# Optimization experiments

Hardware: AMD Instinct MI355X
Metric: run time of the kernel (lower is better)

## Reference

```python
import jax, jax.numpy as jnp
import numpy as np
from jax import lax

B, S, I, H = 128, 256, 512, 1024


def setup_inputs() -> dict:
    key = jax.random.key(0)
    ks = jax.random.split(key, 7)
    s_att = 1.0 / np.sqrt(I + H)
    s_ih = 1.0 / np.sqrt(H)
    return {
        "x": jax.random.normal(ks[0], (B, S, I), dtype=jnp.float32),
        "W_att": jax.random.uniform(ks[1], (1, I + H), minval=-s_att, maxval=s_att, dtype=jnp.float32),
        "b_att": jax.random.uniform(ks[2], (1,), minval=-s_att, maxval=s_att, dtype=jnp.float32),
        "W_ih": jax.random.uniform(ks[3], (3 * H, I), minval=-s_ih, maxval=s_ih, dtype=jnp.float32),
        "W_hh": jax.random.uniform(ks[4], (3 * H, H), minval=-s_ih, maxval=s_ih, dtype=jnp.float32),
        "b_ih": jax.random.uniform(ks[5], (3 * H,), minval=-s_ih, maxval=s_ih, dtype=jnp.float32),
        "b_hh": jax.random.uniform(ks[6], (3 * H,), minval=-s_ih, maxval=s_ih, dtype=jnp.float32),
    }


def reference(x, W_att, b_att, W_ih, W_hh, b_ih, b_hh):
    batch, seq_len, _ = x.shape
    hid = W_hh.shape[1]

    def step(h, x_t):
        # attention score over the BATCH dim (faithful to softmax(dim=0) on [B,1])
        score = jnp.concatenate([x_t, h], axis=1) @ W_att.T + b_att  # [B,1]
        att = jax.nn.softmax(score, axis=0)
        x_att = att * x_t  # [B,I]
        # PyTorch GRUCell: gates in order r, z, n
        gi = x_att @ W_ih.T + b_ih  # [B,3H]
        gh = h @ W_hh.T + b_hh      # [B,3H]
        i_r, i_z, i_n = jnp.split(gi, 3, axis=1)
        h_r, h_z, h_n = jnp.split(gh, 3, axis=1)
        r = jax.nn.sigmoid(i_r + h_r)
        z = jax.nn.sigmoid(i_z + h_z)
        n = jnp.tanh(i_n + r * h_n)
        h_new = (1.0 - z) * n + z * h
        return h_new, h_new

    h0 = jnp.zeros((batch, hid), dtype=x.dtype)
    xs = jnp.swapaxes(x, 0, 1)  # [S,B,I]
    h_last, outs = lax.scan(step, h0, xs)  # outs: [S,B,H]
    outputs = jnp.swapaxes(outs, 0, 1)  # [B,S,H]
    return outputs, h_last
```

## Files before the change

### kernel.cpp

```cpp
#include <hip/hip_runtime.h>
#include <hip/hip_bf16.h>

#define B_ 128
#define S_ 256
#define I_ 512
#define H_ 1024

typedef float  f32x4  __attribute__((ext_vector_type(4)));
typedef __bf16 bf16x8 __attribute__((ext_vector_type(8)));
typedef unsigned short u16x8 __attribute__((ext_vector_type(8)));

__device__ __forceinline__ unsigned short f2bf(float f) {
    unsigned u = __float_as_uint(f);
    unsigned r = (u + 0x7fffu + ((u >> 16) & 1u)) >> 16;
    return (unsigned short)r;
}
__device__ __forceinline__ float bf2f(unsigned short s) {
    return __uint_as_float(((unsigned)s) << 16);
}


__global__ __launch_bounds__(256) void pack_wih(const float* __restrict__ W,
                                                unsigned short* __restrict__ out) {
    int gid = blockIdx.x * 256 + threadIdx.x;
    int lane = gid & 63, ks = (gid >> 6) & 15, p = gid >> 10;
    int c = lane & 15, quad = lane >> 4;
    int k = ks * 32 + quad * 8;
    int n = 0; bool valid = true;
    if (c < 4) n = p * 4 + c;
    else if (c < 8) n = H_ + p * 4 + (c - 4);
    else if (c < 12) n = 2 * H_ + p * 4 + (c - 8);
    else valid = false;
    const float* src = W + (size_t)n * I_ + k;
    u16x8 v;
#pragma unroll
    for (int jj = 0; jj < 8; jj++) v[jj] = valid ? f2bf(src[jj]) : (unsigned short)0;
    *(u16x8*)(out + (size_t)gid * 8) = v;
}

__global__ __launch_bounds__(256) void pack_whh(const float* __restrict__ W,
                                                const float* __restrict__ Watt,
                                                unsigned short* __restrict__ hi,
                                                unsigned short* __restrict__ lo) {
    int gid = blockIdx.x * 256 + threadIdx.x;
    int lane = gid & 63, ks = (gid >> 6) & 31, p = gid >> 11;
    int c = lane & 15, quad = lane >> 4;
    int k = ks * 32 + quad * 8;
    u16x8 vh, vl;
#pragma unroll
    for (int jj = 0; jj < 8; jj++) {
        float f = 0.f;
        if (c < 4)        f = W[(size_t)(p * 4 + c) * H_ + k + jj];
        else if (c < 8)   f = W[(size_t)(H_ + p * 4 + (c - 4)) * H_ + k + jj];
        else if (c < 12)  f = W[(size_t)(2 * H_ + p * 4 + (c - 8)) * H_ + k + jj];
        else if (c == 12) f = Watt[I_ + k + jj];
        unsigned short h16 = f2bf(f);
        unsigned short l16 = f2bf(f - bf2f(h16));
        vh[jj] = h16; vl[jj] = l16;
    }
    *(u16x8*)(hi + (size_t)gid * 8) = vh;
    *(u16x8*)(lo + (size_t)gid * 8) = vl;
}

__global__ __launch_bounds__(256) void pack_x(const float* __restrict__ x,
                                              unsigned short* __restrict__ Gx) {
    int bid = blockIdx.x;
    int t = bid >> 3, m = bid & 7;
    int tid = threadIdx.x;
    __shared__ unsigned short tile[16 * 520];
#pragma unroll
    for (int pass = 0; pass < 8; pass++) {
        int idx = pass * 256 + tid;
        int row = idx >> 7, c4 = idx & 127;
        float4 v = *(const float4*)(x + ((size_t)(m * 16 + row) * S_ + t) * I_ + c4 * 4);
        unsigned short* d = &tile[row * 520 + c4 * 4];
        d[0] = f2bf(v.x); d[1] = f2bf(v.y); d[2] = f2bf(v.z); d[3] = f2bf(v.w);
    }
    __syncthreads();
#pragma unroll
    for (int pass = 0; pass < 4; pass++) {
        int chunk = pass * 256 + tid;
        int ks = chunk >> 6, lane = chunk & 63;
        int c = lane & 15, kq = lane >> 4;
        int k = ks * 32 + kq * 8;
        u16x8 v = *(const u16x8*)(&tile[c * 520 + k]);
        *(u16x8*)(Gx + (((size_t)(t * 8 + m) * 16 + ks) * 64 + lane) * 8) = v;
    }
}

__global__ __launch_bounds__(256) void sx_kernel(const float* __restrict__ x,
                                                 const float* __restrict__ Watt,
                                                 float* __restrict__ sx) {
    int t = blockIdx.x;
    int w = threadIdx.x >> 6, lane = threadIdx.x & 63;
    float4 wa0 = *(const float4*)(Watt + lane * 8);
    float4 wa1 = *(const float4*)(Watt + lane * 8 + 4);
    for (int i = 0; i < 32; i++) {
        int b = w * 32 + i;
        const float4* xp = (const float4*)(x + ((size_t)b * S_ + t) * I_ + lane * 8);
        float4 a0 = xp[0], a1 = xp[1];
        float s = a0.x * wa0.x + a0.y * wa0.y + a0.z * wa0.z + a0.w * wa0.w
                + a1.x * wa1.x + a1.y * wa1.y + a1.z * wa1.z + a1.w * wa1.w;
#pragma unroll
        for (int off = 1; off < 64; off <<= 1) s += __shfl_xor(s, off, 64);
        if (lane == 0) sx[t * 128 + b] = s;
    }
}

__global__ __launch_bounds__(512, 2) void gru_persist(
        const unsigned short* __restrict__ Gx,
        const float* __restrict__ sx,
        const unsigned short* __restrict__ WihP,
        const unsigned short* __restrict__ WhhHiP,
        const unsigned short* __restrict__ WhhLoP,
        unsigned short* __restrict__ Hhi,
        unsigned short* __restrict__ Hlo,
        const float* __restrict__ batt,
        const float* __restrict__ bih, const float* __restrict__ bhh,
        float* __restrict__ out, unsigned* __restrict__ bar) {
    int p = blockIdx.x;
    int tid = threadIdx.x, w = tid >> 6, lane = tid & 63;
    int quad = lane >> 4, c = lane & 15, cl = c & 3;

    __shared__ unsigned short bhi[16384];
    __shared__ unsigned short blo[16384];
    __shared__ unsigned short wih_lds[8192];
    __shared__ float sh_lds[128];
    __shared__ float score_lds[128];

    {
        const uint4* s0 = (const uint4*)(WhhHiP + (size_t)p * 16384);
        uint4* d0 = (uint4*)bhi;
        for (int i = tid; i < 2048; i += 512) d0[i] = s0[i];
        const uint4* s1 = (const uint4*)(WhhLoP + (size_t)p * 16384);
        uint4* d1 = (uint4*)blo;
        for (int i = tid; i < 2048; i += 512) d1[i] = s1[i];
        const uint4* s2 = (const uint4*)(WihP + (size_t)p * 8192);
        uint4* d2 = (uint4*)wih_lds;
        for (int i = tid; i < 1024; i += 512) d2[i] = s2[i];
    }
    float ba = batt[0];
    int j = p * 4 + cl;
    float bihr = bih[j], bihz = bih[H_ + j], bihn = bih[2 * H_ + j];
    float bhhr = bhh[j], bhhz = bhh[H_ + j], bhhn = bhh[2 * H_ + j];
    __syncthreads();

    float hprev[4] = {0.f, 0.f, 0.f, 0.f};
    int k32 = (p & 7) * 4 + cl;
    int j_e = k32 & 7;
    size_t chunk_base = ((size_t)w * 32 + (size_t)(p >> 3)) * 64
                      + (size_t)(quad * 4) + 16 * (size_t)(k32 >> 3);

    for (int t = 0; t < S_; t++) {
        const unsigned short* hchi = Hhi + (size_t)t * 131072;
        const unsigned short* hclo = Hlo + (size_t)t * 131072;
        unsigned* hnhi32 = (unsigned*)(Hhi + (size_t)(t + 1) * 131072);
        unsigned* hnlo32 = (unsigned*)(Hlo + (size_t)(t + 1) * 131072);
        float sxv = (tid < 128) ? sx[t * 128 + tid] : 0.f;

        const unsigned short* ahb = hchi + (size_t)w * 16384 + (size_t)lane * 8;
        const unsigned short* alb = hclo + (size_t)w * 16384 + (size_t)lane * 8;
        const unsigned short* xab = Gx + (size_t)t * 65536 + (size_t)w * 8192
                                       + (size_t)lane * 8;

        u16x8 ph[8], pl8[8], px[8];
#pragma unroll
        for (int s = 0; s < 8; s++) {
            ph[s]  = *(const u16x8*)(ahb + s * 512);
            pl8[s] = *(const u16x8*)(alb + s * 512);
            px[s]  = *(const u16x8*)(xab + s * 512);
        }

        f32x4 accg = (f32x4){0.f, 0.f, 0.f, 0.f};
        f32x4 acc0 = (f32x4){0.f, 0.f, 0.f, 0.f};
        f32x4 acc1 = (f32x4){0.f, 0.f, 0.f, 0.f};
#pragma unroll
        for (int ks = 0; ks < 32; ks++) {
            const int s = ks & 7;
            bf16x8 ah = __builtin_bit_cast(bf16x8, ph[s]);
            bf16x8 al = __builtin_bit_cast(bf16x8, pl8[s]);
            bf16x8 bh = *(const bf16x8*)(bhi + ((size_t)ks * 64 + lane) * 8);
            bf16x8 bl = *(const bf16x8*)(blo + ((size_t)ks * 64 + lane) * 8);
            if (ks < 16) {
                bf16x8 xa = __builtin_bit_cast(bf16x8, px[s]);
                bf16x8 wb = *(const bf16x8*)(wih_lds + ((size_t)ks * 64 + lane) * 8);
                accg = __builtin_amdgcn_mfma_f32_16x16x32_bf16(xa, wb, accg, 0, 0, 0);
                if (ks + 8 < 16) px[s] = *(const u16x8*)(xab + (ks + 8) * 512);
            }
            if (ks & 1) {
                acc1 = __builtin_amdgcn_mfma_f32_16x16x32_bf16(ah, bh, acc1, 0, 0, 0);
                acc1 = __builtin_amdgcn_mfma_f32_16x16x32_bf16(al, bh, acc1, 0, 0, 0);
                acc1 = __builtin_amdgcn_mfma_f32_16x16x32_bf16(ah, bl, acc1, 0, 0, 0);
            } else {
                acc0 = __builtin_amdgcn_mfma_f32_16x16x32_bf16(ah, bh, acc0, 0, 0, 0);
                acc0 = __builtin_amdgcn_mfma_f32_16x16x32_bf16(al, bh, acc0, 0, 0, 0);
                acc0 = __builtin_amdgcn_mfma_f32_16x16x32_bf16(ah, bl, acc0, 0, 0, 0);
            }
            if (ks + 8 < 32) {
                ph[s]  = *(const u16x8*)(ahb + (ks + 8) * 512);
                pl8[s] = *(const u16x8*)(alb + (ks + 8) * 512);
            }
        }

        f32x4 gh;
#pragma unroll
        for (int r = 0; r < 4; r++) gh[r] = acc0[r] + acc1[r];
        if (c == 12) {
#pragma unroll
            for (int r = 0; r < 4; r++) sh_lds[w * 16 + quad * 4 + r] = gh[r];
        }
        __syncthreads();
        if (tid < 128) score_lds[tid] = sh_lds[tid] + sxv + ba;
        __syncthreads();

        float s0 = score_lds[lane], s1 = score_lds[lane + 64];
        float mx = fmaxf(s0, s1);
#pragma unroll
        for (int off = 1; off < 64; off <<= 1) mx = fmaxf(mx, __shfl_xor(mx, off, 64));
        float pe = __expf(s0 - mx) + __expf(s1 - mx);
#pragma unroll
        for (int off = 1; off < 64; off <<= 1) pe += __shfl_xor(pe, off, 64);
        float rden = 1.f / pe;

#pragma unroll
        for (int r = 0; r < 4; r++) {
            int b = w * 16 + quad * 4 + r;
            float att = __expf(score_lds[b] - mx) * rden;
            float ghr = gh[r];
            float ghz = __shfl_xor(ghr, 4, 64);
            float ghn = __shfl_xor(ghr, 8, 64);
            float gir = accg[r];
            float giz = __shfl_xor(gir, 4, 64);
            float gin = __shfl_xor(gir, 8, 64);
            float rg = 1.f / (1.f + __expf(-(att * gir + bihr + ghr + bhhr)));
            float zg = 1.f / (1.f + __expf(-(att * giz + bihz + ghz + bhhz)));
            float ta = att * gin + bihn + rg * (ghn + bhhn);
            ta = fminf(fmaxf(ta, -15.f), 15.f);
            float e2 = __expf(2.f * ta);
            float ng = (e2 - 1.f) / (e2 + 1.f);
            float hnew = (1.f - zg) * ng + zg * hprev[r];
            hprev[r] = hnew;
            if (c < 4) {
                out[((size_t)b * S_ + t) * H_ + j] = hnew;
                unsigned short hi16 = f2bf(hnew);
                unsigned short lo16 = f2bf(hnew - bf2f(hi16));
                unsigned hval = (unsigned)hi16 | ((unsigned)lo16 << 16);
                unsigned nb = __shfl_xor(hval, 1, 64);
                if (!(cl & 1)) {
                    unsigned hipair = (hval & 0xffffu) | (nb << 16);
                    unsigned lopair = (hval >> 16) | (nb & 0xffff0000u);
                    unsigned* dh = hnhi32 + (chunk_base + r) * 4 + (j_e >> 1);
                    unsigned* dl = hnlo32 + (chunk_base + r) * 4 + (j_e >> 1);
                    asm volatile("global_store_dword %0, %1, off sc0 sc1"
                                 :: "v"(dh), "v"(hipair) : "memory");
                    asm volatile("global_store_dword %0, %1, off sc0 sc1"
                                 :: "v"(dl), "v"(lopair) : "memory");
                }
            }
        }

        if (t + 1 < S_) {
            __syncthreads();
            if (tid < 64) {
                if (lane == 0)
                    __hip_atomic_fetch_add(bar + (p & 7) * 32, 1u,
                                           __ATOMIC_RELAXED, __HIP_MEMORY_SCOPE_AGENT);
                unsigned tgt = (unsigned)(t + 1) * 32u;
                for (;;) {
                    unsigned v = tgt;
                    if (lane < 8)
                        v = __hip_atomic_load(bar + lane * 32, __ATOMIC_RELAXED,
                                              __HIP_MEMORY_SCOPE_AGENT);
                    if (__all(v >= tgt)) break;
                    __builtin_amdgcn_s_sleep(1);
                }
            }
            __syncthreads();
        }
    }

    if (c < 4) {
#pragma unroll
        for (int r = 0; r < 4; r++)
            out[(size_t)B_ * S_ * H_ + (size_t)(w * 16 + quad * 4 + r) * H_ + j] = hprev[r];
    }
}

extern "C" void kernel_launch(void* const* d_in, const int* in_sizes, int n_in,
                              void* d_out, int out_size, void* d_ws, size_t ws_size,
                              hipStream_t stream) {
    (void)in_sizes; (void)n_in; (void)out_size; (void)ws_size;
    const float* x    = (const float*)d_in[0];
    const float* Watt = (const float*)d_in[1];
    const float* batt = (const float*)d_in[2];
    const float* Wih  = (const float*)d_in[3];
    const float* Whh  = (const float*)d_in[4];
    const float* bih  = (const float*)d_in[5];
    const float* bhh  = (const float*)d_in[6];
    float* out = (float*)d_out;

    char* ws = (char*)d_ws;
    size_t off = 0;
    unsigned short* Gx     = (unsigned short*)(ws + off); off += 33554432ULL;
    unsigned short* WihP   = (unsigned short*)(ws + off); off += 4194304ULL;
    unsigned short* WhhHiP = (unsigned short*)(ws + off); off += 8388608ULL;
    unsigned short* WhhLoP = (unsigned short*)(ws + off); off += 8388608ULL;
    float*          sx     = (float*)(ws + off);          off += 131072ULL;
    unsigned short* Hhi    = (unsigned short*)(ws + off); off += 67371008ULL;
    unsigned short* Hlo    = (unsigned short*)(ws + off); off += 67371008ULL;
    unsigned*       bar    = (unsigned*)(ws + off);       off += 1024ULL;

    hipMemsetAsync(Hhi, 0, 262144, stream);
    hipMemsetAsync(Hlo, 0, 262144, stream);
    hipMemsetAsync(bar, 0, 1024, stream);
    pack_wih<<<1024, 256, 0, stream>>>(Wih, WihP);
    pack_whh<<<2048, 256, 0, stream>>>(Whh, Watt, WhhHiP, WhhLoP);
    pack_x<<<2048, 256, 0, stream>>>(x, Gx);
    sx_kernel<<<256, 256, 0, stream>>>(x, Watt, sx);
    gru_persist<<<256, 512, 0, stream>>>(Gx, sx, WihP, WhhHiP, WhhLoP, Hhi, Hlo,
                                         batt, bih, bhh, out, bar);
}
```

Measured before the change: 3.264 ms.

## Split recurrent K-loop across two wave groups with 1024-thread blocks

Doubles the block to 1024 threads. The lower 8 waves compute the first half of the W_hh K-reduction, and the upper 8 waves compute the second half plus the input-gate MFMAs. Partial sums are combined through LDS before the softmax and gate epilogue. The next step's x tile and sx value are prefetched after the current step's compute to shorten the serial per-step critical path. The cost is an extra LDS exchange and barrier, higher register pressure from launch_bounds(1024,4), and upper waves sitting idle during the epilogue.

```diff
diff --git a/kernel.cpp b/kernel.cpp
--- a/kernel.cpp
+++ b/kernel.cpp
@@ -107,7 +107,7 @@
     }
 }
 
-__global__ __launch_bounds__(512, 2) void gru_persist(
+__global__ __launch_bounds__(1024, 4) void gru_persist(
         const unsigned short* __restrict__ Gx,
         const float* __restrict__ sx,
         const unsigned short* __restrict__ WihP,
@@ -119,30 +119,36 @@
         const float* __restrict__ bih, const float* __restrict__ bhh,
         float* __restrict__ out, unsigned* __restrict__ bar) {
     int p = blockIdx.x;
-    int tid = threadIdx.x, w = tid >> 6, lane = tid & 63;
+    int tid = threadIdx.x, w16 = tid >> 6, lane = tid & 63;
+    const bool upper = (w16 >= 8);
+    int w = upper ? (w16 - 8) : w16;
     int quad = lane >> 4, c = lane & 15, cl = c & 3;
 
     __shared__ unsigned short bhi[16384];
     __shared__ unsigned short blo[16384];
     __shared__ unsigned short wih_lds[8192];
+    __shared__ f32x4 part_gh[8][64];
+    __shared__ f32x4 part_gi[8][64];
     __shared__ float sh_lds[128];
     __shared__ float score_lds[128];
 
     {
         const uint4* s0 = (const uint4*)(WhhHiP + (size_t)p * 16384);
         uint4* d0 = (uint4*)bhi;
-        for (int i = tid; i < 2048; i += 512) d0[i] = s0[i];
+        for (int i = tid; i < 2048; i += 1024) d0[i] = s0[i];
         const uint4* s1 = (const uint4*)(WhhLoP + (size_t)p * 16384);
         uint4* d1 = (uint4*)blo;
-        for (int i = tid; i < 2048; i += 512) d1[i] = s1[i];
+        for (int i = tid; i < 2048; i += 1024) d1[i] = s1[i];
         const uint4* s2 = (const uint4*)(WihP + (size_t)p * 8192);
-        uint4* d2 = (uint4*)wih_lds;
-        for (int i = tid; i < 1024; i += 512) d2[i] = s2[i];
+        ((uint4*)wih_lds)[tid] = s2[tid];
     }
     float ba = batt[0];
     int j = p * 4 + cl;
-    float bihr = bih[j], bihz = bih[H_ + j], bihn = bih[2 * H_ + j];
-    float bhhr = bhh[j], bhhz = bhh[H_ + j], bhhn = bhh[2 * H_ + j];
+    float bihr = 0.f, bihz = 0.f, bihn = 0.f, bhhr = 0.f, bhhz = 0.f, bhhn = 0.f;
+    if (!upper) {
+        bihr = bih[j]; bihz = bih[H_ + j]; bihn = bih[2 * H_ + j];
+        bhhr = bhh[j]; bhhz = bhh[H_ + j]; bhhn = bhh[2 * H_ + j];
+    }
     __syncthreads();
 
     float hprev[4] = {0.f, 0.f, 0.f, 0.f};
@@ -151,112 +157,170 @@
     size_t chunk_base = ((size_t)w * 32 + (size_t)(p >> 3)) * 64
                       + (size_t)(quad * 4) + 16 * (size_t)(k32 >> 3);
 
+    u16x8 px[8];
+    if (upper) {
+        const unsigned short* xab0 = Gx + (size_t)w * 8192 + (size_t)lane * 8;
+#pragma unroll
+        for (int s = 0; s < 8; s++) px[s] = *(const u16x8*)(xab0 + s * 512);
+    }
+    float sxv = (tid < 128) ? sx[tid] : 0.f;
+
     for (int t = 0; t < S_; t++) {
         const unsigned short* hchi = Hhi + (size_t)t * 131072;
         const unsigned short* hclo = Hlo + (size_t)t * 131072;
         unsigned* hnhi32 = (unsigned*)(Hhi + (size_t)(t + 1) * 131072);
         unsigned* hnlo32 = (unsigned*)(Hlo + (size_t)(t + 1) * 131072);
-        float sxv = (tid < 128) ? sx[t * 128 + tid] : 0.f;
-
-        const unsigned short* ahb = hchi + (size_t)w * 16384 + (size_t)lane * 8;
-        const unsigned short* alb = hclo + (size_t)w * 16384 + (size_t)lane * 8;
-        const unsigned short* xab = Gx + (size_t)t * 65536 + (size_t)w * 8192
-                                       + (size_t)lane * 8;
-
-        u16x8 ph[8], pl8[8], px[8];
-#pragma unroll
-        for (int s = 0; s < 8; s++) {
-            ph[s]  = *(const u16x8*)(ahb + s * 512);
-            pl8[s] = *(const u16x8*)(alb + s * 512);
-            px[s]  = *(const u16x8*)(xab + s * 512);
-        }
-
-        f32x4 accg = (f32x4){0.f, 0.f, 0.f, 0.f};
+
         f32x4 acc0 = (f32x4){0.f, 0.f, 0.f, 0.f};
         f32x4 acc1 = (f32x4){0.f, 0.f, 0.f, 0.f};
-#pragma unroll
-        for (int ks = 0; ks < 32; ks++) {
-            const int s = ks & 7;
-            bf16x8 ah = __builtin_bit_cast(bf16x8, ph[s]);
-            bf16x8 al = __builtin_bit_cast(bf16x8, pl8[s]);
-            bf16x8 bh = *(const bf16x8*)(bhi + ((size_t)ks * 64 + lane) * 8);
-            bf16x8 bl = *(const bf16x8*)(blo + ((size_t)ks * 64 + lane) * 8);
-            if (ks < 16) {
-                bf16x8 xa = __builtin_bit_cast(bf16x8, px[s]);
-                bf16x8 wb = *(const bf16x8*)(wih_lds + ((size_t)ks * 64 + lane) * 8);
+        f32x4 gh;
+
+        if (!upper) {
+            const unsigned short* ahb = hchi + (size_t)w * 16384 + (size_t)lane * 8;
+            const unsigned short* alb = hclo + (size_t)w * 16384 + (size_t)lane * 8;
+            u16x8 ph[8], pl8[8];
+#pragma unroll
+            for (int s = 0; s < 8; s++) {
+                ph[s]  = *(const u16x8*)(ahb + s * 512);
+                pl8[s] = *(const u16x8*)(alb + s * 512);
+            }
+#pragma unroll
+            for (int ks = 0; ks < 16; ks++) {
+                const int s = ks & 7;
+                bf16x8 ah = __builtin_bit_cast(bf16x8, ph[s]);
+                bf16x8 al = __builtin_bit_cast(bf16x8, pl8[s]);
+                bf16x8 bh = *(const bf16x8*)(bhi + ((size_t)ks * 64 + lane) * 8);
+                bf16x8 bl = *(const bf16x8*)(blo + ((size_t)ks * 64 + lane) * 8);
+                if (ks & 1) {
+                    acc1 = __builtin_amdgcn_mfma_f32_16x16x32_bf16(ah, bh, acc1, 0, 0, 0);
+                    acc1 = __builtin_amdgcn_mfma_f32_16x16x32_bf16(al, bh, acc1, 0, 0, 0);
+                    acc1 = __builtin_amdgcn_mfma_f32_16x16x32_bf16(ah, bl, acc1, 0, 0, 0);
+                } else {
+                    acc0 = __builtin_amdgcn_mfma_f32_16x16x32_bf16(ah, bh, acc0, 0, 0, 0);
+                    acc0 = __builtin_amdgcn_mfma_f32_16x16x32_bf16(al, bh, acc0, 0, 0, 0);
+                    acc0 = __builtin_amdgcn_mfma_f32_16x16x32_bf16(ah, bl, acc0, 0, 0, 0);
+                }
+                if (ks < 8) {
+                    ph[s]  = *(const u16x8*)(ahb + (ks + 8) * 512);
+                    pl8[s] = *(const u16x8*)(alb + (ks + 8) * 512);
+                }
+            }
+        } else {
+            const unsigned short* ahb = hchi + (size_t)w * 16384 + (size_t)lane * 8 + 16 * 512;
+            const unsigned short* alb = hclo + (size_t)w * 16384 + (size_t)lane * 8 + 16 * 512;
+            const unsigned short* xab = Gx + (size_t)t * 65536 + (size_t)w * 8192
+                                           + (size_t)lane * 8;
+            f32x4 accg = (f32x4){0.f, 0.f, 0.f, 0.f};
+            u16x8 ph[4], pl8[4];
+#pragma unroll
+            for (int s = 0; s < 4; s++) {
+                ph[s]  = *(const u16x8*)(ahb + s * 512);
+                pl8[s] = *(const u16x8*)(alb + s * 512);
+            }
+#pragma unroll
+            for (int kk = 0; kk < 16; kk++) {
+                const int s = kk & 3;
+                const int ks = 16 + kk;
+                bf16x8 ah = __builtin_bit_cast(bf16x8, ph[s]);
+                bf16x8 al = __builtin_bit_cast(bf16x8, pl8[s]);
+                bf16x8 bh = *(const bf16x8*)(bhi + ((size_t)ks * 64 + lane) * 8);
+                bf16x8 bl = *(const bf16x8*)(blo + ((size_t)ks * 64 + lane) * 8);
+                bf16x8 xa = __builtin_bit_cast(bf16x8, px[kk & 7]);
+                bf16x8 wb = *(const bf16x8*)(wih_lds + ((size_t)kk * 64 + lane) * 8);
                 accg = __builtin_amdgcn_mfma_f32_16x16x32_bf16(xa, wb, accg, 0, 0, 0);
-                if (ks + 8 < 16) px[s] = *(const u16x8*)(xab + (ks + 8) * 512);
-            }
-            if (ks & 1) {
-                acc1 = __builtin_amdgcn_mfma_f32_16x16x32_bf16(ah, bh, acc1, 0, 0, 0);
-                acc1 = __builtin_amdgcn_mfma_f32_16x16x32_bf16(al, bh, acc1, 0, 0, 0);
-                acc1 = __builtin_amdgcn_mfma_f32_16x16x32_bf16(ah, bl, acc1, 0, 0, 0);
-            } else {
-                acc0 = __builtin_amdgcn_mfma_f32_16x16x32_bf16(ah, bh, acc0, 0, 0, 0);
-                acc0 = __builtin_amdgcn_mfma_f32_16x16x32_bf16(al, bh, acc0, 0, 0, 0);
-                acc0 = __builtin_amdgcn_mfma_f32_16x16x32_bf16(ah, bl, acc0, 0, 0, 0);
-            }
-            if (ks + 8 < 32) {
-                ph[s]  = *(const u16x8*)(ahb + (ks + 8) * 512);
-                pl8[s] = *(const u16x8*)(alb + (ks + 8) * 512);
-            }
-        }
-
-        f32x4 gh;
-#pragma unroll
-        for (int r = 0; r < 4; r++) gh[r] = acc0[r] + acc1[r];
-        if (c == 12) {
-#pragma unroll
-            for (int r = 0; r < 4; r++) sh_lds[w * 16 + quad * 4 + r] = gh[r];
+                if (kk & 1) {
+                    acc1 = __builtin_amdgcn_mfma_f32_16x16x32_bf16(ah, bh, acc1, 0, 0, 0);
+                    acc1 = __builtin_amdgcn_mfma_f32_16x16x32_bf16(al, bh, acc1, 0, 0, 0);
+                    acc1 = __builtin_amdgcn_mfma_f32_16x16x32_bf16(ah, bl, acc1, 0, 0, 0);
+                } else {
+                    acc0 = __builtin_amdgcn_mfma_f32_16x16x32_bf16(ah, bh, acc0, 0, 0, 0);
+                    acc0 = __builtin_amdgcn_mfma_f32_16x16x32_bf16(al, bh, acc0, 0, 0, 0);
+                    acc0 = __builtin_amdgcn_mfma_f32_16x16x32_bf16(ah, bl, acc0, 0, 0, 0);
+                }
+                if (kk < 8) px[kk & 7] = *(const u16x8*)(xab + (kk + 8) * 512);
+                if (kk < 12) {
+                    ph[s]  = *(const u16x8*)(ahb + (kk + 4) * 512);
+                    pl8[s] = *(const u16x8*)(alb + (kk + 4) * 512);
+                }
+            }
+            int tn = (t + 1 < S_) ? (t + 1) : t;
+            const unsigned short* xabn = Gx + (size_t)tn * 65536 + (size_t)w * 8192
+                                            + (size_t)lane * 8;
+#pragma unroll
+            for (int s = 0; s < 8; s++) px[s] = *(const u16x8*)(xabn + s * 512);
+            f32x4 gsum;
+#pragma unroll
+            for (int r = 0; r < 4; r++) gsum[r] = acc0[r] + acc1[r];
+            part_gh[w][lane] = gsum;
+            part_gi[w][lane] = accg;
+        }
+        __syncthreads();
+
+        f32x4 pi;
+        if (!upper) {
+            f32x4 pg = part_gh[w][lane];
+            pi = part_gi[w][lane];
+#pragma unroll
+            for (int r = 0; r < 4; r++) gh[r] = acc0[r] + acc1[r] + pg[r];
+            if (c == 12) {
+#pragma unroll
+                for (int r = 0; r < 4; r++) sh_lds[w * 16 + quad * 4 + r] = gh[r];
+            }
         }
         __syncthreads();
         if (tid < 128) score_lds[tid] = sh_lds[tid] + sxv + ba;
         __syncthreads();
 
-        float s0 = score_lds[lane], s1 = score_lds[lane + 64];
-        float mx = fmaxf(s0, s1);
-#pragma unroll
-        for (int off = 1; off < 64; off <<= 1) mx = fmaxf(mx, __shfl_xor(mx, off, 64));
-        float pe = __expf(s0 - mx) + __expf(s1 - mx);
-#pragma unroll
-        for (int off = 1; off < 64; off <<= 1) pe += __shfl_xor(pe, off, 64);
-        float rden = 1.f / pe;
-
-#pragma unroll
-        for (int r = 0; r < 4; r++) {
-            int b = w * 16 + quad * 4 + r;
-            float att = __expf(score_lds[b] - mx) * rden;
-            float ghr = gh[r];
-            float ghz = __shfl_xor(ghr, 4, 64);
-            float ghn = __shfl_xor(ghr, 8, 64);
-            float gir = accg[r];
-            float giz = __shfl_xor(gir, 4, 64);
-            float gin = __shfl_xor(gir, 8, 64);
-            float rg = 1.f / (1.f + __expf(-(att * gir + bihr + ghr + bhhr)));
-            float zg = 1.f / (1.f + __expf(-(att * giz + bihz + ghz + bhhz)));
-            float ta = att * gin + bihn + rg * (ghn + bhhn);
-            ta = fminf(fmaxf(ta, -15.f), 15.f);
-            float e2 = __expf(2.f * ta);
-            float ng = (e2 - 1.f) / (e2 + 1.f);
-            float hnew = (1.f - zg) * ng + zg * hprev[r];
-            hprev[r] = hnew;
-            if (c < 4) {
-                out[((size_t)b * S_ + t) * H_ + j] = hnew;
-                unsigned short hi16 = f2bf(hnew);
-                unsigned short lo16 = f2bf(hnew - bf2f(hi16));
-                unsigned hval = (unsigned)hi16 | ((unsigned)lo16 << 16);
-                unsigned nb = __shfl_xor(hval, 1, 64);
-                if (!(cl & 1)) {
-                    unsigned hipair = (hval & 0xffffu) | (nb << 16);
-                    unsigned lopair = (hval >> 16) | (nb & 0xffff0000u);
-                    unsigned* dh = hnhi32 + (chunk_base + r) * 4 + (j_e >> 1);
-                    unsigned* dl = hnlo32 + (chunk_base + r) * 4 + (j_e >> 1);
-                    asm volatile("global_store_dword %0, %1, off sc0 sc1"
-                                 :: "v"(dh), "v"(hipair) : "memory");
-                    asm volatile("global_store_dword %0, %1, off sc0 sc1"
-                                 :: "v"(dl), "v"(lopair) : "memory");
-                }
-            }
+        if (!upper) {
+            float s0 = score_lds[lane], s1 = score_lds[lane + 64];
+            float mx = fmaxf(s0, s1);
+#pragma unroll
+            for (int off = 1; off < 64; off <<= 1) mx = fmaxf(mx, __shfl_xor(mx, off, 64));
+            float pe = __expf(s0 - mx) + __expf(s1 - mx);
+#pragma unroll
+            for (int off = 1; off < 64; off <<= 1) pe += __shfl_xor(pe, off, 64);
+            float rden = 1.f / pe;
+
+#pragma unroll
+            for (int r = 0; r < 4; r++) {
+                int b = w * 16 + quad * 4 + r;
+                float att = __expf(score_lds[b] - mx) * rden;
+                float ghr = gh[r];
+                float ghz = __shfl_xor(ghr, 4, 64);
+                float ghn = __shfl_xor(ghr, 8, 64);
+                float gir = pi[r];
+                float giz = __shfl_xor(gir, 4, 64);
+                float gin = __shfl_xor(gir, 8, 64);
+                float rg = 1.f / (1.f + __expf(-(att * gir + bihr + ghr + bhhr)));
+                float zg = 1.f / (1.f + __expf(-(att * giz + bihz + ghz + bhhz)));
+                float ta = att * gin + bihn + rg * (ghn + bhhn);
+                ta = fminf(fmaxf(ta, -15.f), 15.f);
+                float e2 = __expf(2.f * ta);
+                float ng = (e2 - 1.f) / (e2 + 1.f);
+                float hnew = (1.f - zg) * ng + zg * hprev[r];
+                hprev[r] = hnew;
+                if (c < 4) {
+                    out[((size_t)b * S_ + t) * H_ + j] = hnew;
+                    unsigned short hi16 = f2bf(hnew);
+                    unsigned short lo16 = f2bf(hnew - bf2f(hi16));
+                    unsigned hval = (unsigned)hi16 | ((unsigned)lo16 << 16);
+                    unsigned nb = __shfl_xor(hval, 1, 64);
+                    if (!(cl & 1)) {
+                        unsigned hipair = (hval & 0xffffu) | (nb << 16);
+                        unsigned lopair = (hval >> 16) | (nb & 0xffff0000u);
+                        unsigned* dh = hnhi32 + (chunk_base + r) * 4 + (j_e >> 1);
+                        unsigned* dl = hnlo32 + (chunk_base + r) * 4 + (j_e >> 1);
+                        asm volatile("global_store_dword %0, %1, off sc0 sc1"
+                                     :: "v"(dh), "v"(hipair) : "memory");
+                        asm volatile("global_store_dword %0, %1, off sc0 sc1"
+                                     :: "v"(dl), "v"(lopair) : "memory");
+                    }
+                }
+            }
+        }
+        if (tid < 128) {
+            int tn = (t + 1 < S_) ? (t + 1) : t;
+            sxv = sx[tn * 128 + tid];
         }
 
         if (t + 1 < S_) {
@@ -279,7 +343,7 @@
         }
     }
 
-    if (c < 4) {
+    if (!upper && c < 4) {
 #pragma unroll
         for (int r = 0; r < 4; r++)
             out[(size_t)B_ * S_ * H_ + (size_t)(w * 16 + quad * 4 + r) * H_ + j] = hprev[r];
@@ -317,6 +381,6 @@
     pack_whh<<<2048, 256, 0, stream>>>(Whh, Watt, WhhHiP, WhhLoP);
     pack_x<<<2048, 256, 0, stream>>>(x, Gx);
     sx_kernel<<<256, 256, 0, stream>>>(x, Watt, sx);
-    gru_persist<<<256, 512, 0, stream>>>(Gx, sx, WihP, WhhHiP, WhhLoP, Hhi, Hlo,
-                                         batt, bih, bhh, out, bar);
-}
+    gru_persist<<<256, 1024, 0, stream>>>(Gx, sx, WihP, WhhHiP, WhhLoP, Hhi, Hlo,
+                                          batt, bih, bhh, out, bar);
+}
```

Measured after the change: 3.687 ms. 13.0% more time.

## Stream H and Gx operands through LDS via async global_load_lds ring buffer

Applied to the files above, without the earlier changes.

Replaces the register-prefetched A operands (h hi/lo and attended x) with a 3-slot per-wave LDS ring filled by global_load_lds, using explicit vmcnt waits so MFMAs overlap the in-flight loads. The softmax over the batch now reduces within each wave by shuffles and combines eight per-wave (max, sum) pairs through LDS, which removes one block barrier per step. The next step's sx values are prefetched into registers. This lowers VGPR pressure (launch bounds relaxed) but adds about 73KB of LDS staging and relies on hand-tuned vmcnt counts that must match the compiler's load ordering.

```diff
diff --git a/kernel.cpp b/kernel.cpp
--- a/kernel.cpp
+++ b/kernel.cpp
@@ -107,7 +107,7 @@
     }
 }
 
-__global__ __launch_bounds__(512, 2) void gru_persist(
+__global__ __launch_bounds__(512) void gru_persist(
         const unsigned short* __restrict__ Gx,
         const float* __restrict__ sx,
         const unsigned short* __restrict__ WihP,
@@ -125,8 +125,8 @@
     __shared__ unsigned short bhi[16384];
     __shared__ unsigned short blo[16384];
     __shared__ unsigned short wih_lds[8192];
-    __shared__ float sh_lds[128];
-    __shared__ float score_lds[128];
+    __shared__ unsigned short hstage[36864];
+    __shared__ float2 swr[8];
 
     {
         const uint4* s0 = (const uint4*)(WhhHiP + (size_t)p * 16384);
@@ -151,24 +151,32 @@
     size_t chunk_base = ((size_t)w * 32 + (size_t)(p >> 3)) * 64
                       + (size_t)(quad * 4) + 16 * (size_t)(k32 >> 3);
 
+    int b0r = w * 16 + quad * 4;
+    unsigned short* stg = hstage + (size_t)w * 4608;
+
+    float sxr[4];
+#pragma unroll
+    for (int r = 0; r < 4; r++) sxr[r] = sx[b0r + r];
+
     for (int t = 0; t < S_; t++) {
-        const unsigned short* hchi = Hhi + (size_t)t * 131072;
-        const unsigned short* hclo = Hlo + (size_t)t * 131072;
+        const unsigned short* hbhi = Hhi + (size_t)t * 131072 + (size_t)w * 16384
+                                         + (size_t)lane * 8;
+        const unsigned short* hblo = Hlo + (size_t)t * 131072 + (size_t)w * 16384
+                                         + (size_t)lane * 8;
+        const unsigned short* xb   = Gx + (size_t)t * 65536 + (size_t)w * 8192
+                                        + (size_t)lane * 8;
         unsigned* hnhi32 = (unsigned*)(Hhi + (size_t)(t + 1) * 131072);
         unsigned* hnlo32 = (unsigned*)(Hlo + (size_t)(t + 1) * 131072);
-        float sxv = (tid < 128) ? sx[t * 128 + tid] : 0.f;
-
-        const unsigned short* ahb = hchi + (size_t)w * 16384 + (size_t)lane * 8;
-        const unsigned short* alb = hclo + (size_t)w * 16384 + (size_t)lane * 8;
-        const unsigned short* xab = Gx + (size_t)t * 65536 + (size_t)w * 8192
-                                       + (size_t)lane * 8;
-
-        u16x8 ph[8], pl8[8], px[8];
-#pragma unroll
-        for (int s = 0; s < 8; s++) {
-            ph[s]  = *(const u16x8*)(ahb + s * 512);
-            pl8[s] = *(const u16x8*)(alb + s * 512);
-            px[s]  = *(const u16x8*)(xab + s * 512);
+
+#pragma unroll
+        for (int k = 0; k < 3; k++) {
+            unsigned short* d = stg + k * 1536;
+            __builtin_amdgcn_global_load_lds((const unsigned int*)(hbhi + k * 512),
+                                             (unsigned int*)(d), 16, 0, 0);
+            __builtin_amdgcn_global_load_lds((const unsigned int*)(hblo + k * 512),
+                                             (unsigned int*)(d + 512), 16, 0, 0);
+            __builtin_amdgcn_global_load_lds((const unsigned int*)(xb + k * 512),
+                                             (unsigned int*)(d + 1024), 16, 0, 0);
         }
 
         f32x4 accg = (f32x4){0.f, 0.f, 0.f, 0.f};
@@ -176,16 +184,22 @@
         f32x4 acc1 = (f32x4){0.f, 0.f, 0.f, 0.f};
 #pragma unroll
         for (int ks = 0; ks < 32; ks++) {
-            const int s = ks & 7;
-            bf16x8 ah = __builtin_bit_cast(bf16x8, ph[s]);
-            bf16x8 al = __builtin_bit_cast(bf16x8, pl8[s]);
+            const int slot = ks % 3;
+            if (ks <= 13)      asm volatile("s_waitcnt vmcnt(6)" ::: "memory");
+            else if (ks == 14) asm volatile("s_waitcnt vmcnt(5)" ::: "memory");
+            else if (ks <= 29) asm volatile("s_waitcnt vmcnt(4)" ::: "memory");
+            else if (ks == 30) asm volatile("s_waitcnt vmcnt(2)" ::: "memory");
+            else               asm volatile("s_waitcnt vmcnt(0)" ::: "memory");
+
+            const unsigned short* sb = stg + slot * 1536;
+            bf16x8 ah = *(const bf16x8*)(sb + (size_t)lane * 8);
+            bf16x8 al = *(const bf16x8*)(sb + 512 + (size_t)lane * 8);
             bf16x8 bh = *(const bf16x8*)(bhi + ((size_t)ks * 64 + lane) * 8);
             bf16x8 bl = *(const bf16x8*)(blo + ((size_t)ks * 64 + lane) * 8);
             if (ks < 16) {
-                bf16x8 xa = __builtin_bit_cast(bf16x8, px[s]);
+                bf16x8 xa = *(const bf16x8*)(sb + 1024 + (size_t)lane * 8);
                 bf16x8 wb = *(const bf16x8*)(wih_lds + ((size_t)ks * 64 + lane) * 8);
                 accg = __builtin_amdgcn_mfma_f32_16x16x32_bf16(xa, wb, accg, 0, 0, 0);
-                if (ks + 8 < 16) px[s] = *(const u16x8*)(xab + (ks + 8) * 512);
             }
             if (ks & 1) {
                 acc1 = __builtin_amdgcn_mfma_f32_16x16x32_bf16(ah, bh, acc1, 0, 0, 0);
@@ -196,36 +210,50 @@
                 acc0 = __builtin_amdgcn_mfma_f32_16x16x32_bf16(al, bh, acc0, 0, 0, 0);
                 acc0 = __builtin_amdgcn_mfma_f32_16x16x32_bf16(ah, bl, acc0, 0, 0, 0);
             }
-            if (ks + 8 < 32) {
-                ph[s]  = *(const u16x8*)(ahb + (ks + 8) * 512);
-                pl8[s] = *(const u16x8*)(alb + (ks + 8) * 512);
+            const int k2 = ks + 3;
+            if (k2 < 32) {
+                unsigned short* d = stg + slot * 1536;
+                __builtin_amdgcn_global_load_lds((const unsigned int*)(hbhi + k2 * 512),
+                                                 (unsigned int*)(d), 16, 0, 0);
+                __builtin_amdgcn_global_load_lds((const unsigned int*)(hblo + k2 * 512),
+                                                 (unsigned int*)(d + 512), 16, 0, 0);
+                if (k2 < 16)
+                    __builtin_amdgcn_global_load_lds((const unsigned int*)(xb + k2 * 512),
+                                                     (unsigned int*)(d + 1024), 16, 0, 0);
             }
         }
 
         f32x4 gh;
 #pragma unroll
         for (int r = 0; r < 4; r++) gh[r] = acc0[r] + acc1[r];
-        if (c == 12) {
-#pragma unroll
-            for (int r = 0; r < 4; r++) sh_lds[w * 16 + quad * 4 + r] = gh[r];
-        }
+
+        float sc[4];
+#pragma unroll
+        for (int r = 0; r < 4; r++) {
+            float shr = __shfl(gh[r], (lane & 0x30) + 12, 64);
+            sc[r] = shr + sxr[r] + ba;
+        }
+        float mw = fmaxf(fmaxf(sc[0], sc[1]), fmaxf(sc[2], sc[3]));
+        mw = fmaxf(mw, __shfl_xor(mw, 16, 64));
+        mw = fmaxf(mw, __shfl_xor(mw, 32, 64));
+        float ew = __expf(sc[0] - mw) + __expf(sc[1] - mw)
+                 + __expf(sc[2] - mw) + __expf(sc[3] - mw);
+        ew += __shfl_xor(ew, 16, 64);
+        ew += __shfl_xor(ew, 32, 64);
+        if (lane == 0) swr[w] = (float2){mw, ew};
         __syncthreads();
-        if (tid < 128) score_lds[tid] = sh_lds[tid] + sxv + ba;
-        __syncthreads();
-
-        float s0 = score_lds[lane], s1 = score_lds[lane + 64];
-        float mx = fmaxf(s0, s1);
-#pragma unroll
-        for (int off = 1; off < 64; off <<= 1) mx = fmaxf(mx, __shfl_xor(mx, off, 64));
-        float pe = __expf(s0 - mx) + __expf(s1 - mx);
-#pragma unroll
-        for (int off = 1; off < 64; off <<= 1) pe += __shfl_xor(pe, off, 64);
+        float mx = swr[0].x;
+#pragma unroll
+        for (int i = 1; i < 8; i++) mx = fmaxf(mx, swr[i].x);
+        float pe = 0.f;
+#pragma unroll
+        for (int i = 0; i < 8; i++) pe += swr[i].y * __expf(swr[i].x - mx);
         float rden = 1.f / pe;
 
 #pragma unroll
         for (int r = 0; r < 4; r++) {
-            int b = w * 16 + quad * 4 + r;
-            float att = __expf(score_lds[b] - mx) * rden;
+            int b = b0r + r;
+            float att = __expf(sc[r] - mx) * rden;
             float ghr = gh[r];
             float ghz = __shfl_xor(ghr, 4, 64);
             float ghn = __shfl_xor(ghr, 8, 64);
@@ -259,6 +287,12 @@
             }
         }
 
+        {
+            int tn = (t + 1 < S_) ? (t + 1) : t;
+#pragma unroll
+            for (int r = 0; r < 4; r++) sxr[r] = sx[tn * 128 + b0r + r];
+        }
+
         if (t + 1 < S_) {
             __syncthreads();
             if (tid < 64) {
@@ -282,7 +316,7 @@
     if (c < 4) {
 #pragma unroll
         for (int r = 0; r < 4; r++)
-            out[(size_t)B_ * S_ * H_ + (size_t)(w * 16 + quad * 4 + r) * H_ + j] = hprev[r];
+            out[(size_t)B_ * S_ * H_ + (size_t)(b0r + r) * H_ + j] = hprev[r];
     }
 }
 
```

After: 3.088 ms. 5.4% less time.
